# Performance work log

Hardware: AMD Instinct MI355X
Metric: run time of the kernel (lower is better)

## Reference

```python
import jax, jax.numpy as jnp
import numpy as np

B, T, C = 4, 2048, 1024
H = 16
D = C // H  # 64


def setup_inputs() -> dict:
    key = jax.random.key(0)
    ks = jax.random.split(key, 3)
    scale = 1.0 / np.sqrt(C)
    return {
        "x": jax.random.normal(ks[0], (B, T, C), dtype=jnp.float32),
        "W_attn": jax.random.normal(ks[1], (C, 3 * C), dtype=jnp.float32) * scale,
        "b_attn": jnp.zeros((3 * C,), dtype=jnp.float32),
        "W_proj": jax.random.normal(ks[2], (C, C), dtype=jnp.float32) * scale,
        "b_proj": jnp.zeros((C,), dtype=jnp.float32),
    }


def reference(x, W_attn, b_attn, W_proj, b_proj):
    b, t, c = x.shape
    qkv = x @ W_attn + b_attn                      # [B,T,3C]
    q, k, v = jnp.split(qkv, 3, axis=-1)           # each [B,T,C]
    to_heads = lambda z: z.reshape(b, t, H, D).transpose(0, 2, 1, 3)  # [B,H,T,D]
    q, k, v = to_heads(q), to_heads(k), to_heads(v)
    scores = jnp.einsum("bhtd,bhsd->bhts", q, k) / jnp.sqrt(jnp.float32(D))
    causal = jnp.tril(jnp.ones((t, t), dtype=bool))  # [T,T]
    scores = jnp.where(causal[None, None], scores, jnp.finfo(scores.dtype).min)
    attn = jax.nn.softmax(scores, axis=-1)           # [B,H,T,T]
    out = jnp.einsum("bhts,bhsd->bhtd", attn, v)     # [B,H,T,D]
    out = out.transpose(0, 2, 1, 3).reshape(b, t, c)
    return out @ W_proj + b_proj
```

## Files before the change

### kernel.cpp

```cpp
#include <hip/hip_runtime.h>
#include <hip/hip_bf16.h>

typedef __bf16 bf16_t;
typedef __attribute__((ext_vector_type(8))) __bf16 bf16x8;
typedef __attribute__((ext_vector_type(4))) float f32x4;
typedef __attribute__((ext_vector_type(4))) unsigned short u16x4;
typedef __attribute__((ext_vector_type(4))) unsigned int u32x4;

#define B_DIM 4
#define T_DIM 2048
#define C_DIM 1024
#define H_DIM 16
#define D_DIM 64
#define M_TOK (B_DIM * T_DIM)
#define N_QKV (3 * C_DIM)
#define NT    (T_DIM / 64)
#define KSTR  72
#define TILE_E (64 * KSTR)
#define CSC   0.18033688011112042f

__device__ __forceinline__ void gload_lds16(const bf16_t* g, bf16_t* l) {
  __builtin_amdgcn_global_load_lds((const __attribute__((address_space(1))) void*)(g),
                                   (__attribute__((address_space(3))) void*)(l), 16, 0, 0);
}

__global__ void cvt_f32_to_bf16(const float* __restrict__ in, bf16_t* __restrict__ out, int n4) {
  int i = blockIdx.x * blockDim.x + threadIdx.x;
  if (i >= n4) return;
  float4 v = ((const float4*)in)[i];
  struct alignas(8) bv4 { bf16_t x, y, z, w; };
  bv4 o;
  o.x = (bf16_t)v.x; o.y = (bf16_t)v.y; o.z = (bf16_t)v.z; o.w = (bf16_t)v.w;
  ((bv4*)out)[i] = o;
}

__global__ void transpose_f32_to_bf16(const float* __restrict__ in, bf16_t* __restrict__ out,
                                      int K, int N) {
  __shared__ float tile[32][33];
  int bx = blockIdx.x * 32;
  int by = blockIdx.y * 32;
  int tx = threadIdx.x, ty = threadIdx.y;
#pragma unroll
  for (int i = 0; i < 32; i += 8)
    tile[ty + i][tx] = in[(size_t)(by + ty + i) * N + bx + tx];
  __syncthreads();
#pragma unroll
  for (int i = 0; i < 32; i += 8)
    out[(size_t)(bx + ty + i) * K + by + tx] = (bf16_t)tile[tx][ty + i];
}

template <typename OutT>
__global__ __launch_bounds__(512, 2)
void gemm256(const bf16_t* __restrict__ A, const bf16_t* __restrict__ Bt,
             const float* __restrict__ bias, OutT* __restrict__ C,
             int M, int N, int K) {
  __shared__ alignas(16) bf16_t As[3][256 * 64];
  __shared__ alignas(16) bf16_t Bs[3][128 * 64];

  const int tid = threadIdx.x;
  const int lane = tid & 63;
  const int w = tid >> 6;
  const int w8 = w * 8;
  const int quad = lane >> 4, l16 = lane & 15;
  const int wrow = (w >> 1) * 64;
  const int wcol = (w & 1) * 64;
  const int row0 = blockIdx.x * 256, col0 = blockIdx.y * 128;

  const int lrow = lane >> 3;
  const int sw = ((lane & 7) ^ (lrow & 7)) * 8;
  const bf16_t* Ag = A + (size_t)(row0 + w8 + lrow) * K + sw;
  const bf16_t* Bg = Bt + (size_t)(col0 + w8 + lrow) * K + sw;

  const int NTK = K >> 6;

#define STAGE_TILE(tt, bi)                                                     \
  do {                                                                         \
    const size_t ko = (size_t)(tt) * 64;                                       \
    _Pragma("unroll")                                                          \
    for (int c = 0; c < 4; ++c)                                                \
      gload_lds16(Ag + ko + (size_t)(c * 64) * K, &As[bi][(c * 64 + w8) * 64]);\
    _Pragma("unroll")                                                          \
    for (int c = 0; c < 2; ++c)                                                \
      gload_lds16(Bg + ko + (size_t)(c * 64) * K, &Bs[bi][(c * 64 + w8) * 64]);\
  } while (0)

  f32x4 acc[4][4];
#pragma unroll
  for (int i = 0; i < 4; ++i)
#pragma unroll
    for (int j = 0; j < 4; ++j)
      acc[i][j] = (f32x4){0.f, 0.f, 0.f, 0.f};

  STAGE_TILE(0, 0);
  if (1 < NTK) STAGE_TILE(1, 1);

  for (int t = 0; t < NTK; ++t) {
    const int cur = t % 3;
    asm volatile("s_barrier" ::: "memory");
    if (t + 2 < NTK) {
      STAGE_TILE(t + 2, (t + 2) % 3);
      __builtin_amdgcn_sched_barrier(0);
      asm volatile("s_waitcnt vmcnt(12)" ::: "memory");
    } else if (t + 1 < NTK) {
      asm volatile("s_waitcnt vmcnt(6)" ::: "memory");
    } else {
      asm volatile("s_waitcnt vmcnt(0)" ::: "memory");
    }
    __builtin_amdgcn_sched_barrier(0);
    asm volatile("s_barrier" ::: "memory");

    const bf16_t* AsT = &As[cur][0];
    const bf16_t* BsT = &Bs[cur][0];
#pragma unroll
    for (int kk = 0; kk < 2; ++kk) {
      bf16x8 af[4], bfr[4];
      const int sl = (kk * 4 + quad) ^ (l16 & 7);
#pragma unroll
      for (int i = 0; i < 4; ++i)
        af[i] = *(const bf16x8*)&AsT[(wrow + i * 16 + l16) * 64 + sl * 8];
#pragma unroll
      for (int j = 0; j < 4; ++j)
        bfr[j] = *(const bf16x8*)&BsT[(wcol + j * 16 + l16) * 64 + sl * 8];
      __builtin_amdgcn_s_setprio(1);
#pragma unroll
      for (int i = 0; i < 4; ++i)
#pragma unroll
        for (int j = 0; j < 4; ++j)
          acc[i][j] = __builtin_amdgcn_mfma_f32_16x16x32_bf16(af[i], bfr[j], acc[i][j], 0, 0, 0);
      __builtin_amdgcn_s_setprio(0);
    }
  }
#undef STAGE_TILE

#pragma unroll
  for (int i = 0; i < 4; ++i)
#pragma unroll
    for (int j = 0; j < 4; ++j) {
      int col = col0 + wcol + j * 16 + l16;
      float bv = bias[col];
#pragma unroll
      for (int r = 0; r < 4; ++r) {
        int row = row0 + wrow + i * 16 + quad * 4 + r;
        C[(size_t)row * N + col] = (OutT)(acc[i][j][r] + bv);
      }
    }
}

__global__ __launch_bounds__(256, 4)
void attn_fwd(const bf16_t* __restrict__ qkv, bf16_t* __restrict__ out) {
  __shared__ alignas(16) bf16_t Ks[2][TILE_E];
  __shared__ alignas(16) bf16_t Vt[2][TILE_E];

  const int tid = threadIdx.x;
  const int lane = tid & 63;
  const int wave = tid >> 6;
  const int quad = lane >> 4, l16 = lane & 15;
  const int qlo = blockIdx.x;
  const int qhi = NT - 1 - qlo;
  const int h = blockIdx.y, b = blockIdx.z;
  const size_t tokBase = (size_t)b * T_DIM;

  const bf16_t* qpl = qkv + (tokBase + qlo * 64 + wave * 16 + l16) * N_QKV + h * D_DIM;
  const bf16_t* qph = qkv + (tokBase + qhi * 64 + wave * 16 + l16) * N_QKV + h * D_DIM;
  bf16x8 ql0 = *(const bf16x8*)(qpl + quad * 8);
  bf16x8 ql1 = *(const bf16x8*)(qpl + 32 + quad * 8);
  bf16x8 qh0 = *(const bf16x8*)(qph + quad * 8);
  bf16x8 qh1 = *(const bf16x8*)(qph + 32 + quad * 8);

  f32x4 ol[4], oh[4];
#pragma unroll
  for (int dt = 0; dt < 4; ++dt) {
    ol[dt] = (f32x4){0.f, 0.f, 0.f, 0.f};
    oh[dt] = (f32x4){0.f, 0.f, 0.f, 0.f};
  }
  float ll = 0.f, lh = 0.f;

  const int tx = tid & 15, ty = tid >> 4;
  const int vswz = ((tx >> 2) & 3) * 8;
  const int vcol = (8 * (ty & 3) + 4 * ((ty >> 2) & 1) + 32 * (ty >> 3)) ^ vswz;
  const f32x4 zero4 = (f32x4){0.f, 0.f, 0.f, 0.f};

  u16x4 kreg[4], vreg[4];
  const bf16_t* kb0 = qkv + (tokBase + ty * 4) * N_QKV + h * D_DIM + C_DIM + tx * 4;
#pragma unroll
  for (int r = 0; r < 4; ++r) kreg[r] = *(const u16x4*)(kb0 + (size_t)r * N_QKV);
#pragma unroll
  for (int r = 0; r < 4; ++r) vreg[r] = *(const u16x4*)(kb0 + (size_t)r * N_QKV + C_DIM);
#pragma unroll
  for (int r = 0; r < 4; ++r)
    *(u16x4*)&Ks[0][(ty * 4 + r) * KSTR + tx * 4] = kreg[r];
#pragma unroll
  for (int i = 0; i < 4; ++i) {
    u16x4 p = (u16x4){vreg[0][i], vreg[1][i], vreg[2][i], vreg[3][i]};
    *(u16x4*)&Vt[0][(tx * 4 + i) * KSTR + vcol] = p;
  }
  __syncthreads();

  for (int t = 0; t <= qhi; ++t) {
    const int cur = t & 1;
    const bool lo = (t <= qlo);

    if (t < qhi) {
      const bf16_t* kb = qkv + (tokBase + (t + 1) * 64 + ty * 4) * N_QKV + h * D_DIM + C_DIM + tx * 4;
#pragma unroll
      for (int r = 0; r < 4; ++r) kreg[r] = *(const u16x4*)(kb + (size_t)r * N_QKV);
#pragma unroll
      for (int r = 0; r < 4; ++r) vreg[r] = *(const u16x4*)(kb + (size_t)r * N_QKV + C_DIM);
    }

    f32x4 svl[4], svh[4];
    __builtin_amdgcn_s_setprio(1);
#pragma unroll
    for (int ct = 0; ct < 4; ++ct) {
      bf16x8 kf0 = *(const bf16x8*)&Ks[cur][(ct * 16 + l16) * KSTR + quad * 8];
      bf16x8 kf1 = *(const bf16x8*)&Ks[cur][(ct * 16 + l16) * KSTR + 32 + quad * 8];
      if (lo) {
        svl[ct] = __builtin_amdgcn_mfma_f32_16x16x32_bf16(kf0, ql0, zero4, 0, 0, 0);
        svl[ct] = __builtin_amdgcn_mfma_f32_16x16x32_bf16(kf1, ql1, svl[ct], 0, 0, 0);
      }
      svh[ct] = __builtin_amdgcn_mfma_f32_16x16x32_bf16(kf0, qh0, zero4, 0, 0, 0);
      svh[ct] = __builtin_amdgcn_mfma_f32_16x16x32_bf16(kf1, qh1, svh[ct], 0, 0, 0);
    }
    __builtin_amdgcn_s_setprio(0);
    if (t == qlo) {
      const int qr = wave * 16 + l16;
#pragma unroll
      for (int ct = 0; ct < 4; ++ct)
#pragma unroll
        for (int r = 0; r < 4; ++r)
          if (ct * 16 + quad * 4 + r > qr) svl[ct][r] = -INFINITY;
    }
    if (t == qhi) {
      const int qr = wave * 16 + l16;
#pragma unroll
      for (int ct = 0; ct < 4; ++ct)
#pragma unroll
        for (int r = 0; r < 4; ++r)
          if (ct * 16 + quad * 4 + r > qr) svh[ct][r] = -INFINITY;
    }

    struct alignas(4) bpair { bf16_t lo, hi; };
    bf16x8 pl0, pl1, ph0, ph1;
    if (lo) {
      float rsum = 0.f;
      unsigned int lw[8];
#pragma unroll
      for (int ct = 0; ct < 4; ++ct) {
        float e0 = __builtin_amdgcn_exp2f(svl[ct][0] * CSC);
        float e1 = __builtin_amdgcn_exp2f(svl[ct][1] * CSC);
        float e2 = __builtin_amdgcn_exp2f(svl[ct][2] * CSC);
        float e3 = __builtin_amdgcn_exp2f(svl[ct][3] * CSC);
        rsum += (e0 + e1) + (e2 + e3);
        bpair w0 = {(bf16_t)e0, (bf16_t)e1};
        bpair w1 = {(bf16_t)e2, (bf16_t)e3};
        lw[ct * 2 + 0] = __builtin_bit_cast(unsigned int, w0);
        lw[ct * 2 + 1] = __builtin_bit_cast(unsigned int, w1);
      }
      rsum += __shfl_xor(rsum, 16);
      rsum += __shfl_xor(rsum, 32);
      ll += rsum;
      u32x4 pw0 = (u32x4){lw[0], lw[1], lw[2], lw[3]};
      u32x4 pw1 = (u32x4){lw[4], lw[5], lw[6], lw[7]};
      pl0 = __builtin_bit_cast(bf16x8, pw0);
      pl1 = __builtin_bit_cast(bf16x8, pw1);
    }
    {
      float rsum = 0.f;
      unsigned int lw[8];
#pragma unroll
      for (int ct = 0; ct < 4; ++ct) {
        float e0 = __builtin_amdgcn_exp2f(svh[ct][0] * CSC);
        float e1 = __builtin_amdgcn_exp2f(svh[ct][1] * CSC);
        float e2 = __builtin_amdgcn_exp2f(svh[ct][2] * CSC);
        float e3 = __builtin_amdgcn_exp2f(svh[ct][3] * CSC);
        rsum += (e0 + e1) + (e2 + e3);
        bpair w0 = {(bf16_t)e0, (bf16_t)e1};
        bpair w1 = {(bf16_t)e2, (bf16_t)e3};
        lw[ct * 2 + 0] = __builtin_bit_cast(unsigned int, w0);
        lw[ct * 2 + 1] = __builtin_bit_cast(unsigned int, w1);
      }
      rsum += __shfl_xor(rsum, 16);
      rsum += __shfl_xor(rsum, 32);
      lh += rsum;
      u32x4 pw0 = (u32x4){lw[0], lw[1], lw[2], lw[3]};
      u32x4 pw1 = (u32x4){lw[4], lw[5], lw[6], lw[7]};
      ph0 = __builtin_bit_cast(bf16x8, pw0);
      ph1 = __builtin_bit_cast(bf16x8, pw1);
    }

    if (t < qhi) {
#pragma unroll
      for (int r = 0; r < 4; ++r)
        *(u16x4*)&Ks[cur ^ 1][(ty * 4 + r) * KSTR + tx * 4] = kreg[r];
#pragma unroll
      for (int i = 0; i < 4; ++i) {
        u16x4 p = (u16x4){vreg[0][i], vreg[1][i], vreg[2][i], vreg[3][i]};
        *(u16x4*)&Vt[cur ^ 1][(tx * 4 + i) * KSTR + vcol] = p;
      }
    }

    __builtin_amdgcn_s_setprio(1);
#pragma unroll
    for (int dt = 0; dt < 4; ++dt) {
      const int vc = (quad * 8) ^ (dt * 8);
      bf16x8 vf0 = *(const bf16x8*)&Vt[cur][(dt * 16 + l16) * KSTR + vc];
      bf16x8 vf1 = *(const bf16x8*)&Vt[cur][(dt * 16 + l16) * KSTR + 32 + vc];
      if (lo) {
        ol[dt] = __builtin_amdgcn_mfma_f32_16x16x32_bf16(vf0, pl0, ol[dt], 0, 0, 0);
        ol[dt] = __builtin_amdgcn_mfma_f32_16x16x32_bf16(vf1, pl1, ol[dt], 0, 0, 0);
      }
      oh[dt] = __builtin_amdgcn_mfma_f32_16x16x32_bf16(vf0, ph0, oh[dt], 0, 0, 0);
      oh[dt] = __builtin_amdgcn_mfma_f32_16x16x32_bf16(vf1, ph1, oh[dt], 0, 0, 0);
    }
    __builtin_amdgcn_s_setprio(0);

    __syncthreads();
  }

  struct alignas(8) bh4 { bf16_t a, b, c, d; };
  {
    float rl = 1.0f / ll;
    bf16_t* op = out + (tokBase + qlo * 64 + wave * 16 + l16) * C_DIM + h * D_DIM;
#pragma unroll
    for (int dt = 0; dt < 4; ++dt) {
      bh4 v = {(bf16_t)(ol[dt][0] * rl), (bf16_t)(ol[dt][1] * rl),
               (bf16_t)(ol[dt][2] * rl), (bf16_t)(ol[dt][3] * rl)};
      *(bh4*)(op + dt * 16 + quad * 4) = v;
    }
  }
  {
    float rl = 1.0f / lh;
    bf16_t* op = out + (tokBase + qhi * 64 + wave * 16 + l16) * C_DIM + h * D_DIM;
#pragma unroll
    for (int dt = 0; dt < 4; ++dt) {
      bh4 v = {(bf16_t)(oh[dt][0] * rl), (bf16_t)(oh[dt][1] * rl),
               (bf16_t)(oh[dt][2] * rl), (bf16_t)(oh[dt][3] * rl)};
      *(bh4*)(op + dt * 16 + quad * 4) = v;
    }
  }
}

extern "C" void kernel_launch(void* const* d_in, const int* in_sizes, int n_in,
                              void* d_out, int out_size, void* d_ws, size_t ws_size,
                              hipStream_t stream) {
  const float* x      = (const float*)d_in[0];
  const float* W_attn = (const float*)d_in[1];
  const float* b_attn = (const float*)d_in[2];
  const float* W_proj = (const float*)d_in[3];
  const float* b_proj = (const float*)d_in[4];
  float* out = (float*)d_out;

  char* ws = (char*)d_ws;
  bf16_t* xb   = (bf16_t*)ws;  ws += (size_t)M_TOK * C_DIM * 2;
  bf16_t* Wat  = (bf16_t*)ws;  ws += (size_t)N_QKV * C_DIM * 2;
  bf16_t* Wpt  = (bf16_t*)ws;  ws += (size_t)C_DIM * C_DIM * 2;
  bf16_t* qkv  = (bf16_t*)ws;  ws += (size_t)M_TOK * N_QKV * 2;
  bf16_t* attn = (bf16_t*)ws;  ws += (size_t)M_TOK * C_DIM * 2;

  {
    int n4 = (M_TOK * C_DIM) / 4;
    cvt_f32_to_bf16<<<n4 / 256, 256, 0, stream>>>(x, xb, n4);
  }
  transpose_f32_to_bf16<<<dim3(N_QKV / 32, C_DIM / 32), dim3(32, 8), 0, stream>>>(W_attn, Wat, C_DIM, N_QKV);
  transpose_f32_to_bf16<<<dim3(C_DIM / 32, C_DIM / 32), dim3(32, 8), 0, stream>>>(W_proj, Wpt, C_DIM, C_DIM);

  gemm256<bf16_t><<<dim3(M_TOK / 256, N_QKV / 128), 512, 0, stream>>>(
      xb, Wat, b_attn, qkv, M_TOK, N_QKV, C_DIM);

  attn_fwd<<<dim3(NT / 2, H_DIM, B_DIM), 256, 0, stream>>>(qkv, attn);

  gemm256<float><<<dim3(M_TOK / 256, C_DIM / 128), 512, 0, stream>>>(
      attn, Wpt, b_proj, out, M_TOK, C_DIM, C_DIM);
}
```

Before: 283.5 us.

## Switch GEMMs to 256x256 block tiles with double-buffered LDS staging

Both GEMMs now use a square 256x256 output tile per 512-thread block instead of 256x128. Each wave computes a 128x64 sub-tile with 8x4 MFMA accumulators, which raises arithmetic intensity per LDS load. The LDS pipeline drops from triple to double buffering so the larger tiles fit in shared memory. The cost is far fewer blocks (128 for the output projection on a 256-CU device), heavier register and LDS use per block that limits occupancy, and less latency hiding from the shallower prefetch.

Measured after the change: 289.4 us. 2.1% more time.

```diff
diff --git a/kernel.cpp b/kernel.cpp
--- a/kernel.cpp
+++ b/kernel.cpp
@@ -51,89 +51,86 @@
 
 template <typename OutT>
 __global__ __launch_bounds__(512, 2)
-void gemm256(const bf16_t* __restrict__ A, const bf16_t* __restrict__ Bt,
-             const float* __restrict__ bias, OutT* __restrict__ C,
-             int M, int N, int K) {
-  __shared__ alignas(16) bf16_t As[3][256 * 64];
-  __shared__ alignas(16) bf16_t Bs[3][128 * 64];
+void gemm256sq(const bf16_t* __restrict__ A, const bf16_t* __restrict__ Bt,
+               const float* __restrict__ bias, OutT* __restrict__ C,
+               int M, int N, int K) {
+  __shared__ alignas(16) bf16_t As[2][256 * 64];
+  __shared__ alignas(16) bf16_t Bs[2][256 * 64];
 
   const int tid = threadIdx.x;
   const int lane = tid & 63;
   const int w = tid >> 6;
+  const int quad = lane >> 4, l16 = lane & 15;
+  const int wrow = (w >> 2) * 128;
+  const int wcol = (w & 3) * 64;
+  const int row0 = blockIdx.x * 256, col0 = blockIdx.y * 256;
+
+  const int srow = tid >> 3;
+  const int sw = ((tid & 7) ^ (srow & 7)) * 8;
+  const bf16_t* Ag = A + (size_t)(row0 + srow) * K + sw;
+  const bf16_t* Bg = Bt + (size_t)(col0 + srow) * K + sw;
   const int w8 = w * 8;
-  const int quad = lane >> 4, l16 = lane & 15;
-  const int wrow = (w >> 1) * 64;
-  const int wcol = (w & 1) * 64;
-  const int row0 = blockIdx.x * 256, col0 = blockIdx.y * 128;
-
-  const int lrow = lane >> 3;
-  const int sw = ((lane & 7) ^ (lrow & 7)) * 8;
-  const bf16_t* Ag = A + (size_t)(row0 + w8 + lrow) * K + sw;
-  const bf16_t* Bg = Bt + (size_t)(col0 + w8 + lrow) * K + sw;
 
   const int NTK = K >> 6;
 
-#define STAGE_TILE(tt, bi)                                                     \
-  do {                                                                         \
-    const size_t ko = (size_t)(tt) * 64;                                       \
-    _Pragma("unroll")                                                          \
-    for (int c = 0; c < 4; ++c)                                                \
-      gload_lds16(Ag + ko + (size_t)(c * 64) * K, &As[bi][(c * 64 + w8) * 64]);\
-    _Pragma("unroll")                                                          \
-    for (int c = 0; c < 2; ++c)                                                \
-      gload_lds16(Bg + ko + (size_t)(c * 64) * K, &Bs[bi][(c * 64 + w8) * 64]);\
+#define STG(tt, bi)                                                             \
+  do {                                                                          \
+    const size_t ko = (size_t)(tt) * 64;                                        \
+    _Pragma("unroll")                                                           \
+    for (int c = 0; c < 4; ++c)                                                 \
+      gload_lds16(Ag + ko + (size_t)(c * 64) * K, &As[bi][(c * 64 + w8) * 64]); \
+    _Pragma("unroll")                                                           \
+    for (int c = 0; c < 4; ++c)                                                 \
+      gload_lds16(Bg + ko + (size_t)(c * 64) * K, &Bs[bi][(c * 64 + w8) * 64]); \
   } while (0)
 
-  f32x4 acc[4][4];
-#pragma unroll
-  for (int i = 0; i < 4; ++i)
+  f32x4 acc[8][4];
+#pragma unroll
+  for (int i = 0; i < 8; ++i)
 #pragma unroll
     for (int j = 0; j < 4; ++j)
       acc[i][j] = (f32x4){0.f, 0.f, 0.f, 0.f};
 
-  STAGE_TILE(0, 0);
-  if (1 < NTK) STAGE_TILE(1, 1);
+  STG(0, 0);
 
   for (int t = 0; t < NTK; ++t) {
-    const int cur = t % 3;
-    asm volatile("s_barrier" ::: "memory");
-    if (t + 2 < NTK) {
-      STAGE_TILE(t + 2, (t + 2) % 3);
+    const int cur = t & 1;
+    __builtin_amdgcn_s_barrier();
+    if (t + 1 < NTK) {
+      STG(t + 1, cur ^ 1);
       __builtin_amdgcn_sched_barrier(0);
-      asm volatile("s_waitcnt vmcnt(12)" ::: "memory");
-    } else if (t + 1 < NTK) {
-      asm volatile("s_waitcnt vmcnt(6)" ::: "memory");
+      asm volatile("s_waitcnt vmcnt(8)" ::: "memory");
     } else {
       asm volatile("s_waitcnt vmcnt(0)" ::: "memory");
     }
     __builtin_amdgcn_sched_barrier(0);
-    asm volatile("s_barrier" ::: "memory");
+    __builtin_amdgcn_s_barrier();
 
     const bf16_t* AsT = &As[cur][0];
     const bf16_t* BsT = &Bs[cur][0];
 #pragma unroll
     for (int kk = 0; kk < 2; ++kk) {
-      bf16x8 af[4], bfr[4];
       const int sl = (kk * 4 + quad) ^ (l16 & 7);
-#pragma unroll
-      for (int i = 0; i < 4; ++i)
+      bf16x8 af[8], bfr[4];
+#pragma unroll
+      for (int i = 0; i < 8; ++i)
         af[i] = *(const bf16x8*)&AsT[(wrow + i * 16 + l16) * 64 + sl * 8];
 #pragma unroll
       for (int j = 0; j < 4; ++j)
         bfr[j] = *(const bf16x8*)&BsT[(wcol + j * 16 + l16) * 64 + sl * 8];
       __builtin_amdgcn_s_setprio(1);
 #pragma unroll
-      for (int i = 0; i < 4; ++i)
+      for (int i = 0; i < 8; ++i)
 #pragma unroll
         for (int j = 0; j < 4; ++j)
           acc[i][j] = __builtin_amdgcn_mfma_f32_16x16x32_bf16(af[i], bfr[j], acc[i][j], 0, 0, 0);
       __builtin_amdgcn_s_setprio(0);
     }
   }
-#undef STAGE_TILE
-
-#pragma unroll
-  for (int i = 0; i < 4; ++i)
+#undef STG
+
+#pragma unroll
+  for (int i = 0; i < 8; ++i)
 #pragma unroll
     for (int j = 0; j < 4; ++j) {
       int col = col0 + wcol + j * 16 + l16;
@@ -364,11 +361,11 @@
   transpose_f32_to_bf16<<<dim3(N_QKV / 32, C_DIM / 32), dim3(32, 8), 0, stream>>>(W_attn, Wat, C_DIM, N_QKV);
   transpose_f32_to_bf16<<<dim3(C_DIM / 32, C_DIM / 32), dim3(32, 8), 0, stream>>>(W_proj, Wpt, C_DIM, C_DIM);
 
-  gemm256<bf16_t><<<dim3(M_TOK / 256, N_QKV / 128), 512, 0, stream>>>(
+  gemm256sq<bf16_t><<<dim3(M_TOK / 256, N_QKV / 256), 512, 0, stream>>>(
       xb, Wat, b_attn, qkv, M_TOK, N_QKV, C_DIM);
 
   attn_fwd<<<dim3(NT / 2, H_DIM, B_DIM), 256, 0, stream>>>(qkv, attn);
 
-  gemm256<float><<<dim3(M_TOK / 256, C_DIM / 128), 512, 0, stream>>>(
+  gemm256sq<float><<<dim3(M_TOK / 256, C_DIM / 256), 512, 0, stream>>>(
       attn, Wpt, b_proj, out, M_TOK, C_DIM, C_DIM);
 }
```
